# Kernel tuning notes

Measured on AMD Instinct MI355X. Metric: run time of the kernel, lower is better.

The kernel has to match this reference:

```python
import jax, jax.numpy as jnp
import numpy as np

N = 50000      # nodes
E = 800000     # edges (avg degree 16)
D = 128        # enc_input_dim
H = 4          # enc_num_heads
C = 32         # enc_hidden_dim (per head)
OUT = 64       # linear_output_dim
NEG_SLOPE = 0.2


def setup_inputs() -> dict:
    key = jax.random.key(0)
    ks = jax.random.split(key, 12)
    def glorot(k, shape, fan):
        return (jax.random.normal(k, shape, jnp.float32) / np.sqrt(fan)).astype(jnp.float32)
    x = jax.random.normal(ks[0], (N, D), jnp.float32)
    edge_index = jax.random.randint(ks[1], (2, E), 0, N, dtype=jnp.int64)
    # GAT layer 0: in=D, out=C per head, heads=H, concat -> H*C
    W0 = glorot(ks[2], (D, H * C), D)
    att_src0 = glorot(ks[3], (H, C), C)
    att_dst0 = glorot(ks[4], (H, C), C)
    b0 = jnp.zeros((H * C,), jnp.float32)
    # GAT layer 1: in=H*C, out=D, heads=1
    W1 = glorot(ks[5], (H * C, D), H * C)
    att_src1 = glorot(ks[6], (1, D), D)
    att_dst1 = glorot(ks[7], (1, D), D)
    b1 = jnp.zeros((D,), jnp.float32)
    # projection heads
    Wn = glorot(ks[8], (D, OUT), D)
    bn = jnp.zeros((OUT,), jnp.float32)
    We = glorot(ks[9], (D, OUT), D)
    be = jnp.zeros((OUT,), jnp.float32)
    return dict(x=x, edge_index=edge_index,
                W0=W0, att_src0=att_src0, att_dst0=att_dst0, b0=b0,
                W1=W1, att_src1=att_src1, att_dst1=att_dst1, b1=b1,
                Wn=Wn, bn=bn, We=We, be=be)


def gat_conv(x, src, dst, W, att_s, att_d, b):
    # PyG GATConv: project, per-head attention logits, LeakyReLU,
    # softmax over incoming edges per destination node, scatter-add aggregate.
    n = x.shape[0]
    heads, ch = att_s.shape
    xl = (x @ W).reshape(n, heads, ch)                       # [N,H,C]
    a_s = jnp.einsum('nhc,hc->nh', xl, att_s)                # [N,H]
    a_d = jnp.einsum('nhc,hc->nh', xl, att_d)                # [N,H]
    alpha = jax.nn.leaky_relu(a_s[src] + a_d[dst], NEG_SLOPE)  # [E',H]
    amax = jax.lax.stop_gradient(jax.ops.segment_max(alpha, dst, num_segments=n))
    ex = jnp.exp(alpha - amax[dst])
    denom = jax.ops.segment_sum(ex, dst, num_segments=n)
    w = ex / (denom[dst] + 1e-16)                            # [E',H]
    out = jax.ops.segment_sum(xl[src] * w[:, :, None], dst, num_segments=n)
    return out.reshape(n, heads * ch) + b


def reference(x, edge_index, W0, att_src0, att_dst0, b0,
              W1, att_src1, att_dst1, b1, Wn, bn, We, be):
    n = x.shape[0]
    loop = jnp.arange(n, dtype=edge_index.dtype)             # PyG add_self_loops
    src = jnp.concatenate([edge_index[0], loop])
    dst = jnp.concatenate([edge_index[1], loop])
    h = jax.nn.relu(gat_conv(x, src, dst, W0, att_src0, att_dst0, b0))
    h = jax.nn.relu(gat_conv(h, src, dst, W1, att_src1, att_dst1, b1))
    h_neighbor = h @ Wn + bn
    h_ego = x @ We + be
    return (h_ego, h_neighbor)
```

## Files before the change

kernel.cpp:

```cpp
#include <hip/hip_runtime.h>


#define LEAKY_SLOPE 0.2f
#define BUCKET_CAP 64

typedef __attribute__((ext_vector_type(8))) short s16x8;
typedef __attribute__((ext_vector_type(4))) float f32x4;
typedef __attribute__((ext_vector_type(2))) float f32x2;

static __device__ __forceinline__ unsigned short f2bf(float f)
{
    unsigned x = __float_as_uint(f);
    unsigned r = (x + 0x7fffu + ((x >> 16) & 1u)) >> 16;
    return (unsigned short)r;
}
static __device__ __forceinline__ float bfhi(unsigned u) { return __uint_as_float(u & 0xffff0000u); }
static __device__ __forceinline__ float bflo(unsigned u) { return __uint_as_float(u << 16); }
static __device__ __forceinline__ unsigned char f2fp8(float f)
{
    return (unsigned char)(__builtin_amdgcn_cvt_pk_fp8_f32(f, f, 0, false) & 0xff);
}

__global__ __launch_bounds__(256) void init_k(const float* __restrict__ W0,
                                              const float* __restrict__ W1,
                                              const float* __restrict__ Wn,
                                              const float* __restrict__ We,
                                              unsigned short* __restrict__ P0,
                                              unsigned short* __restrict__ P1,
                                              unsigned short* __restrict__ Pn,
                                              unsigned short* __restrict__ Pe)
{
    int idx = blockIdx.x * 256 + threadIdx.x;
    if (idx < 49152) {
        const float* S; unsigned short* D; int BN; int local;
        if (idx < 16384)      { S = W0; D = P0; BN = 128; local = idx; }
        else if (idx < 32768) { S = W1; D = P1; BN = 128; local = idx - 16384; }
        else if (idx < 40960) { S = Wn; D = Pn; BN = 64;  local = idx - 32768; }
        else                  { S = We; D = Pe; BN = 64;  local = idx - 40960; }
        int k = local / BN, nn = local % BN;
        D[(((k >> 3) * BN + nn) * 8) + (k & 7)] = f2bf(S[local]);
    }
}

static __device__ __forceinline__ void gemm128_body(int tile,
                                                    const float* __restrict__ Ab,
                                                    const unsigned short* __restrict__ Bp,
                                                    unsigned char* __restrict__ Cb,
                                                    const float* __restrict__ ats,
                                                    const float* __restrict__ atd,
                                                    float* __restrict__ a_s,
                                                    float* __restrict__ a_d, int n,
                                                    char* __restrict__ sm)
{
    constexpr int BN = 128;
    constexpr int APITCH = 144;
    constexpr int BPITCH = BN + 2;

    unsigned short* As = (unsigned short*)sm;
    unsigned short* Bs = (unsigned short*)(sm + 64 * APITCH * 2);

    const int t  = threadIdx.x;
    const int rb = tile * 64;

#pragma unroll
    for (int i = 0; i < 4; ++i) {
        int q = t + i * 256;
        int r = q >> 4;
        int c = (q & 15) * 8;
        int gr = rb + r;
        uint4 o = make_uint4(0u, 0u, 0u, 0u);
        if (gr < n) {
            const float* src = Ab + (size_t)gr * 128 + c;
            float4 v0 = *(const float4*)src;
            float4 v1 = *(const float4*)(src + 4);
            o.x = (unsigned)f2bf(v0.x) | ((unsigned)f2bf(v0.y) << 16);
            o.y = (unsigned)f2bf(v0.z) | ((unsigned)f2bf(v0.w) << 16);
            o.z = (unsigned)f2bf(v1.x) | ((unsigned)f2bf(v1.y) << 16);
            o.w = (unsigned)f2bf(v1.z) | ((unsigned)f2bf(v1.w) << 16);
        }
        *(uint4*)(As + r * APITCH + c) = o;
    }
#pragma unroll
    for (int i = 0; i < 8; ++i) {
        int ge = t + i * 256;
        int o = ge / BN, nn = ge % BN;
        *(float4*)(Bs + ((size_t)o * BPITCH + nn) * 8) = *(const float4*)(Bp + (size_t)ge * 8);
    }
    __syncthreads();

    const int w = t >> 6, lane = t & 63;
    const int m = lane & 15, quad = lane >> 4;
    const int wc = w & 1, wr = w >> 1;
    const int row0 = wr * 32;
    const int col0 = wc * 64;

    f32x4 acc[2][4];
#pragma unroll
    for (int rt = 0; rt < 2; ++rt)
#pragma unroll
        for (int c = 0; c < 4; ++c) acc[rt][c] = (f32x4){0.f, 0.f, 0.f, 0.f};

    s16x8 a[2][4];
#pragma unroll
    for (int rt = 0; rt < 2; ++rt)
#pragma unroll
        for (int kk = 0; kk < 4; ++kk)
            a[rt][kk] = *(const s16x8*)(As + (row0 + rt * 16 + m) * APITCH + kk * 32 + quad * 8);

#pragma unroll
    for (int kk = 0; kk < 4; ++kk)
#pragma unroll
        for (int c = 0; c < 4; ++c) {
            s16x8 b = *(const s16x8*)(Bs + ((size_t)(kk * 4 + quad) * BPITCH + col0 + c * 16 + m) * 8);
#pragma unroll
            for (int rt = 0; rt < 2; ++rt)
                acc[rt][c] = __builtin_amdgcn_mfma_f32_16x16x32_bf16(a[rt][kk], b, acc[rt][c], 0, 0, 0);
        }

#pragma unroll
    for (int rt = 0; rt < 2; ++rt)
#pragma unroll
        for (int c = 0; c < 4; ++c)
#pragma unroll
            for (int r = 0; r < 4; ++r) {
                int row = rb + row0 + rt * 16 + quad * 4 + r;
                int colg = col0 + c * 16 + m;
                if (row < n) Cb[(size_t)row * 128 + colg] = f2fp8(acc[rt][c][r]);
            }

    float atsv[4], atdv[4];
#pragma unroll
    for (int c = 0; c < 4; ++c) {
        atsv[c] = ats[col0 + c * 16 + m];
        atdv[c] = atd[col0 + c * 16 + m];
    }
#pragma unroll
    for (int rt = 0; rt < 2; ++rt)
#pragma unroll
        for (int r = 0; r < 4; ++r)
#pragma unroll
            for (int hb = 0; hb < 2; ++hb) {
                float ps = acc[rt][2*hb][r] * atsv[2*hb] + acc[rt][2*hb+1][r] * atsv[2*hb+1];
                float pd = acc[rt][2*hb][r] * atdv[2*hb] + acc[rt][2*hb+1][r] * atdv[2*hb+1];
#pragma unroll
                for (int off = 1; off < 16; off <<= 1) {
                    ps += __shfl_xor(ps, off);
                    pd += __shfl_xor(pd, off);
                }
                int row = rb + row0 + rt * 16 + quad * 4 + r;
                if (m == 0 && row < n) {
                    a_s[(size_t)row * 4 + 2*wc + hb] = ps;
                    a_d[(size_t)row * 4 + 2*wc + hb] = pd;
                }
            }
}

static __device__ __forceinline__ void proj64_body(int tile,
                                                   const float* __restrict__ Ab,
                                                   const unsigned short* __restrict__ Bp,
                                                   const float* __restrict__ bias,
                                                   float* __restrict__ Cf, int n,
                                                   char* __restrict__ sm)
{
    constexpr int BN = 64;
    constexpr int APITCH = 144;
    constexpr int BPITCH = BN + 2;

    unsigned short* As = (unsigned short*)sm;
    unsigned short* Bs = (unsigned short*)(sm + 64 * APITCH * 2);

    const int t  = threadIdx.x;
    const int rb = tile * 64;

#pragma unroll
    for (int i = 0; i < 4; ++i) {
        int q = t + i * 256;
        int r = q >> 4;
        int c = (q & 15) * 8;
        int gr = rb + r;
        uint4 o = make_uint4(0u, 0u, 0u, 0u);
        if (gr < n) {
            const float* src = Ab + (size_t)gr * 128 + c;
            float4 v0 = *(const float4*)src;
            float4 v1 = *(const float4*)(src + 4);
            o.x = (unsigned)f2bf(v0.x) | ((unsigned)f2bf(v0.y) << 16);
            o.y = (unsigned)f2bf(v0.z) | ((unsigned)f2bf(v0.w) << 16);
            o.z = (unsigned)f2bf(v1.x) | ((unsigned)f2bf(v1.y) << 16);
            o.w = (unsigned)f2bf(v1.z) | ((unsigned)f2bf(v1.w) << 16);
        }
        *(uint4*)(As + r * APITCH + c) = o;
    }
#pragma unroll
    for (int i = 0; i < 4; ++i) {
        int ge = t + i * 256;
        int o = ge / BN, nn = ge % BN;
        *(float4*)(Bs + ((size_t)o * BPITCH + nn) * 8) = *(const float4*)(Bp + (size_t)ge * 8);
    }
    __syncthreads();

    const int w = t >> 6, lane = t & 63;
    const int m = lane & 15, quad = lane >> 4;
    const int row0 = w * 16;

    f32x4 acc[4];
#pragma unroll
    for (int c = 0; c < 4; ++c) acc[c] = (f32x4){0.f, 0.f, 0.f, 0.f};

    s16x8 a[4];
#pragma unroll
    for (int kk = 0; kk < 4; ++kk)
        a[kk] = *(const s16x8*)(As + (row0 + m) * APITCH + kk * 32 + quad * 8);

#pragma unroll
    for (int kk = 0; kk < 4; ++kk)
#pragma unroll
        for (int c = 0; c < 4; ++c) {
            s16x8 b = *(const s16x8*)(Bs + ((size_t)(kk * 4 + quad) * BPITCH + c * 16 + m) * 8);
            acc[c] = __builtin_amdgcn_mfma_f32_16x16x32_bf16(a[kk], b, acc[c], 0, 0, 0);
        }

#pragma unroll
    for (int c = 0; c < 4; ++c)
#pragma unroll
        for (int r = 0; r < 4; ++r) {
            int row = rb + row0 + quad * 4 + r;
            int colg = c * 16 + m;
            if (row < n) Cf[(size_t)row * BN + colg] = acc[c][r] + bias[colg];
        }
}

__global__ __launch_bounds__(256) void build_k(const float* __restrict__ x,
                                               const unsigned short* __restrict__ P0,
                                               const unsigned short* __restrict__ Pe,
                                               unsigned char* __restrict__ xlb,
                                               const float* __restrict__ ats,
                                               const float* __restrict__ atd,
                                               float* __restrict__ a_s,
                                               float* __restrict__ a_d,
                                               const float* __restrict__ be,
                                               float* __restrict__ Ce,
                                               const int* __restrict__ ei,
                                               int* __restrict__ curs,
                                               unsigned short* __restrict__ col,
                                               int E, int n,
                                               int scatBlocks, int gemmBlocks)
{
    extern __shared__ char sm[];
    int b = blockIdx.x;
    if (b < scatBlocks) {
        int t8 = (b * 256 + threadIdx.x) * 8;
        if (t8 < E) {
            if ((E & 7) == 0) {
                int4 s0 = *(const int4*)(ei + t8);
                int4 s1 = *(const int4*)(ei + t8 + 4);
                int4 d0 = *(const int4*)(ei + E + t8);
                int4 d1 = *(const int4*)(ei + E + t8 + 4);
                int p0 = atomicAdd(&curs[d0.x << 4], 1);
                int p1 = atomicAdd(&curs[d0.y << 4], 1);
                int p2 = atomicAdd(&curs[d0.z << 4], 1);
                int p3 = atomicAdd(&curs[d0.w << 4], 1);
                int p4 = atomicAdd(&curs[d1.x << 4], 1);
                int p5 = atomicAdd(&curs[d1.y << 4], 1);
                int p6 = atomicAdd(&curs[d1.z << 4], 1);
                int p7 = atomicAdd(&curs[d1.w << 4], 1);
                if (p0 < BUCKET_CAP) col[(d0.x << 6) + p0] = (unsigned short)s0.x;
                if (p1 < BUCKET_CAP) col[(d0.y << 6) + p1] = (unsigned short)s0.y;
                if (p2 < BUCKET_CAP) col[(d0.z << 6) + p2] = (unsigned short)s0.z;
                if (p3 < BUCKET_CAP) col[(d0.w << 6) + p3] = (unsigned short)s0.w;
                if (p4 < BUCKET_CAP) col[(d1.x << 6) + p4] = (unsigned short)s1.x;
                if (p5 < BUCKET_CAP) col[(d1.y << 6) + p5] = (unsigned short)s1.y;
                if (p6 < BUCKET_CAP) col[(d1.z << 6) + p6] = (unsigned short)s1.z;
                if (p7 < BUCKET_CAP) col[(d1.w << 6) + p7] = (unsigned short)s1.w;
            } else {
                int lim = (t8 + 8 < E) ? t8 + 8 : E;
                for (int e = t8; e < lim; ++e) {
                    int s = ei[e], d = ei[E + e];
                    int p = atomicAdd(&curs[d << 4], 1);
                    if (p < BUCKET_CAP) col[(d << 6) + p] = (unsigned short)s;
                }
            }
        }
    } else if (b < scatBlocks + gemmBlocks) {
        gemm128_body(b - scatBlocks, x, P0, xlb, ats, atd, a_s, a_d, n, sm);
    } else {
        proj64_body(b - scatBlocks - gemmBlocks, x, Pe, be, Ce, n, sm);
    }
}

template<int LAYER>
__global__ __launch_bounds__(256) void agg_mv_k(const unsigned char* __restrict__ xin,
                                                const float* __restrict__ asi,
                                                const float* __restrict__ adi,
                                                const int* __restrict__ curs,
                                                const unsigned short* __restrict__ col,
                                                const float* __restrict__ bpre,
                                                const unsigned short* __restrict__ Wp,
                                                const float* __restrict__ ats,
                                                const float* __restrict__ atd,
                                                unsigned char* __restrict__ xlo,
                                                float* __restrict__ aso,
                                                float* __restrict__ ado,
                                                const float* __restrict__ bpost,
                                                float* __restrict__ outf,
                                                int n)
{
    constexpr int H  = (LAYER == 0) ? 4 : 1;
    constexpr int BN = (LAYER == 0) ? 128 : 64;

    __shared__ unsigned short hrow[16 * 128];
    __shared__ float smS[64], smD[64];

    const int t = threadIdx.x;

    const int nd   = t >> 4;
    const int L16  = t & 15;
    const int lane = t & 63;
    const int gb   = lane & 48;
    const int node = blockIdx.x * 16 + nd;
    const int h    = (LAYER == 0) ? (L16 >> 2) : 0;

    if (node < n) {
        float c0=0.f,c1=0.f,c2=0.f,c3=0.f,c4=0.f,c5=0.f,c6=0.f,c7=0.f,den=0.f;
        float ad = adi[(size_t)node * H + h];
        int m = curs[node << 4];
        if (m > BUCKET_CAP) m = BUCKET_CAP;
        const unsigned char* xbase = xin + L16 * 8;
        const int p0 = node << 6;

        int cvu = 0;
        for (int j = 0; j < m; j += 8) {
            if ((j & 15) == 0) cvu = col[p0 + j + L16];
            int cnt = m - j; if (cnt > 8) cnt = 8;
            int sq[8]; float as8[8]; uint2 uv[8];
#pragma unroll
            for (int q = 0; q < 8; ++q) {
                int idx = (q < cnt) ? (j + q) : j;
                sq[q] = __shfl(cvu, gb + (idx & 15));
            }
#pragma unroll
            for (int q = 0; q < 8; ++q) as8[q] = asi[(size_t)sq[q] * H + h];
#pragma unroll
            for (int q = 0; q < 8; ++q) uv[q] = *(const uint2*)(xbase + (size_t)sq[q] * 128);
#pragma unroll
            for (int q = 0; q < 8; ++q) {
                float al = as8[q] + ad;
                al = (al >= 0.f) ? al : LEAKY_SLOPE * al;
                float wq = (q < cnt) ? __expf(al) : 0.f;
                f32x2 pa = __builtin_amdgcn_cvt_pk_f32_fp8((int)uv[q].x, false);
                f32x2 pb = __builtin_amdgcn_cvt_pk_f32_fp8((int)uv[q].x, true);
                f32x2 pc = __builtin_amdgcn_cvt_pk_f32_fp8((int)uv[q].y, false);
                f32x2 pd2 = __builtin_amdgcn_cvt_pk_f32_fp8((int)uv[q].y, true);
                c0 = fmaf(wq, pa[0], c0); c1 = fmaf(wq, pa[1], c1);
                c2 = fmaf(wq, pb[0], c2); c3 = fmaf(wq, pb[1], c3);
                c4 = fmaf(wq, pc[0], c4); c5 = fmaf(wq, pc[1], c5);
                c6 = fmaf(wq, pd2[0], c6); c7 = fmaf(wq, pd2[1], c7);
                den += wq;
            }
        }
        {
            float sv = asi[(size_t)node * H + h];
            float al = sv + ad;
            al = (al >= 0.f) ? al : LEAKY_SLOPE * al;
            float ws = __expf(al);
            uint2 uvs = *(const uint2*)(xbase + (size_t)node * 128);
            f32x2 pa = __builtin_amdgcn_cvt_pk_f32_fp8((int)uvs.x, false);
            f32x2 pb = __builtin_amdgcn_cvt_pk_f32_fp8((int)uvs.x, true);
            f32x2 pc = __builtin_amdgcn_cvt_pk_f32_fp8((int)uvs.y, false);
            f32x2 pd2 = __builtin_amdgcn_cvt_pk_f32_fp8((int)uvs.y, true);
            c0 = fmaf(ws, pa[0], c0); c1 = fmaf(ws, pa[1], c1);
            c2 = fmaf(ws, pb[0], c2); c3 = fmaf(ws, pb[1], c3);
            c4 = fmaf(ws, pc[0], c4); c5 = fmaf(ws, pc[1], c5);
            c6 = fmaf(ws, pd2[0], c6); c7 = fmaf(ws, pd2[1], c7);
            den += ws;
        }
        float inv = 1.0f / (den + 1e-16f);
        const float* bp = bpre + L16 * 8;
        float h0v = fmaxf(fmaf(c0, inv, bp[0]), 0.f);
        float h1v = fmaxf(fmaf(c1, inv, bp[1]), 0.f);
        float h2v = fmaxf(fmaf(c2, inv, bp[2]), 0.f);
        float h3v = fmaxf(fmaf(c3, inv, bp[3]), 0.f);
        float h4v = fmaxf(fmaf(c4, inv, bp[4]), 0.f);
        float h5v = fmaxf(fmaf(c5, inv, bp[5]), 0.f);
        float h6v = fmaxf(fmaf(c6, inv, bp[6]), 0.f);
        float h7v = fmaxf(fmaf(c7, inv, bp[7]), 0.f);
        uint4 hv;
        hv.x = (unsigned)f2bf(h0v) | ((unsigned)f2bf(h1v) << 16);
        hv.y = (unsigned)f2bf(h2v) | ((unsigned)f2bf(h3v) << 16);
        hv.z = (unsigned)f2bf(h4v) | ((unsigned)f2bf(h5v) << 16);
        hv.w = (unsigned)f2bf(h6v) | ((unsigned)f2bf(h7v) << 16);
        *(uint4*)(hrow + nd * 128 + L16 * 8) = hv;
    } else {
        *(uint4*)(hrow + nd * 128 + L16 * 8) = make_uint4(0u, 0u, 0u, 0u);
    }

    __syncthreads();

    const int w    = t >> 6;
    const int m16  = lane & 15;
    const int quad = lane >> 4;

    s16x8 afr[4];
#pragma unroll
    for (int kk = 0; kk < 4; ++kk)
        afr[kk] = *(const s16x8*)(hrow + m16 * 128 + kk * 32 + quad * 8);

    if (LAYER == 0) {
        f32x4 acc[2];
        acc[0] = (f32x4){0.f, 0.f, 0.f, 0.f};
        acc[1] = (f32x4){0.f, 0.f, 0.f, 0.f};
#pragma unroll
        for (int kk = 0; kk < 4; ++kk)
#pragma unroll
            for (int ct = 0; ct < 2; ++ct) {
                int colg = (w * 2 + ct) * 16 + m16;
                s16x8 b = *(const s16x8*)(Wp + ((size_t)(kk * 4 + quad) * BN + colg) * 8);
                acc[ct] = __builtin_amdgcn_mfma_f32_16x16x32_bf16(afr[kk], b, acc[ct], 0, 0, 0);
            }
#pragma unroll
        for (int r = 0; r < 4; ++r) {
            int gnode = blockIdx.x * 16 + quad * 4 + r;
            float ps = 0.f, pd = 0.f;
#pragma unroll
            for (int ct = 0; ct < 2; ++ct) {
                int colg = (w * 2 + ct) * 16 + m16;
                float v = acc[ct][r];
                if (gnode < n) xlo[(size_t)gnode * 128 + colg] = f2fp8(v);
                ps = fmaf(v, ats[colg], ps);
                pd = fmaf(v, atd[colg], pd);
            }
#pragma unroll
            for (int off = 1; off < 16; off <<= 1) {
                ps += __shfl_xor(ps, off);
                pd += __shfl_xor(pd, off);
            }
            if (m16 == 0) {
                smS[(quad * 4 + r) * 4 + w] = ps;
                smD[(quad * 4 + r) * 4 + w] = pd;
            }
        }
        __syncthreads();
        if (t < 16) {
            int gnode = blockIdx.x * 16 + t;
            if (gnode < n) {
                aso[gnode] = smS[t * 4] + smS[t * 4 + 1] + smS[t * 4 + 2] + smS[t * 4 + 3];
                ado[gnode] = smD[t * 4] + smD[t * 4 + 1] + smD[t * 4 + 2] + smD[t * 4 + 3];
            }
        }
    } else {
        f32x4 acc = (f32x4){0.f, 0.f, 0.f, 0.f};
        int colg = w * 16 + m16;
#pragma unroll
        for (int kk = 0; kk < 4; ++kk) {
            s16x8 b = *(const s16x8*)(Wp + ((size_t)(kk * 4 + quad) * BN + colg) * 8);
            acc = __builtin_amdgcn_mfma_f32_16x16x32_bf16(afr[kk], b, acc, 0, 0, 0);
        }
        float bv = bpost[colg];
#pragma unroll
        for (int r = 0; r < 4; ++r) {
            int gnode = blockIdx.x * 16 + quad * 4 + r;
            if (gnode < n) outf[(size_t)gnode * 64 + colg] = acc[r] + bv;
        }
    }
}

extern "C" void kernel_launch(void* const* d_in, const int* in_sizes, int n_in,
                              void* d_out, int out_size, void* d_ws, size_t ws_size,
                              hipStream_t stream)
{
    const float* x   = (const float*)d_in[0];
    const int*   ei  = (const int*)d_in[1];
    const float* W0  = (const float*)d_in[2];
    const float* as0 = (const float*)d_in[3];
    const float* ad0 = (const float*)d_in[4];
    const float* b0  = (const float*)d_in[5];
    const float* W1  = (const float*)d_in[6];
    const float* as1 = (const float*)d_in[7];
    const float* ad1 = (const float*)d_in[8];
    const float* b1  = (const float*)d_in[9];
    const float* Wn  = (const float*)d_in[10];
    const float* bn  = (const float*)d_in[11];
    const float* We  = (const float*)d_in[12];
    const float* be  = (const float*)d_in[13];

    const int n  = in_sizes[0] / 128;
    const int E  = in_sizes[1] / 2;
    float* out = (float*)d_out;

    char* w = (char*)d_ws;
    auto carve = [&](size_t bytes) -> void* {
        void* p = (void*)w;
        w += (bytes + 255) & ~(size_t)255;
        return p;
    };
    unsigned char* xlb = (unsigned char*)carve((size_t)n * 128);
    unsigned char* hb  = (unsigned char*)carve((size_t)n * 128);
    float* a_s0 = (float*)carve((size_t)n * 4 * 4);
    float* a_d0 = (float*)carve((size_t)n * 4 * 4);
    float* a_s1 = (float*)carve((size_t)n * 4);
    float* a_d1 = (float*)carve((size_t)n * 4);
    int*   curs = (int*)carve((size_t)n * 16 * 4);
    unsigned short* colv = (unsigned short*)carve((size_t)n * BUCKET_CAP * 2);
    unsigned short* P0 = (unsigned short*)carve(16384 * 2);
    unsigned short* P1 = (unsigned short*)carve(16384 * 2);
    unsigned short* Pn = (unsigned short*)carve(8192 * 2);
    unsigned short* Pe = (unsigned short*)carve(8192 * 2);

    const int gN64  = (n + 63) / 64;
    const int gB16  = (n + 15) / 16;
    const int gScat = ((E + 7) / 8 + 255) / 256;

    constexpr int GEMM_SM = 64 * 144 * 2 + 16 * 130 * 8 * 2;

    hipMemsetAsync(curs, 0, (size_t)n * 16 * 4, stream);
    init_k<<<192, 256, 0, stream>>>(W0, W1, Wn, We, P0, P1, Pn, Pe);

    build_k<<<gScat + 2 * gN64, 256, GEMM_SM, stream>>>(x, P0, Pe, xlb, as0, ad0,
                                                        a_s0, a_d0, be, out,
                                                        ei, curs, colv, E, n,
                                                        gScat, gN64);

    agg_mv_k<0><<<gB16, 256, 0, stream>>>(xlb, a_s0, a_d0, curs, colv, b0,
                                          P1, as1, ad1,
                                          hb, a_s1, a_d1,
                                          nullptr, nullptr, n);

    agg_mv_k<1><<<gB16, 256, 0, stream>>>(hb, a_s1, a_d1, curs, colv, b1,
                                          Pn, nullptr, nullptr,
                                          nullptr, nullptr, nullptr,
                                          bn, out + (size_t)n * 64, n);
}
```

Baseline: 201.9 us.

## Recompute attention logits from fp8 features in aggregation and drop init kernel

Removes the separate weight-packing kernel. W0/We are now converted to bf16 directly inside the GEMM tile loads, and W1/Wn packing moves into extra blocks of build_k. The per-node a_s/a_d attention arrays are dropped: the aggregation kernel recomputes both logits from the gathered fp8 feature rows with per-lane dot products and shuffle reductions. This saves a launch and the a_s/a_d stores and gathers, but adds ALU and shuffle work per edge and computes logits from fp8-quantized features, which changes precision.

```diff
diff --git a/kernel.cpp b/kernel.cpp
--- a/kernel.cpp
+++ b/kernel.cpp
@@ -14,43 +14,25 @@
     unsigned r = (x + 0x7fffu + ((x >> 16) & 1u)) >> 16;
     return (unsigned short)r;
 }
-static __device__ __forceinline__ float bfhi(unsigned u) { return __uint_as_float(u & 0xffff0000u); }
-static __device__ __forceinline__ float bflo(unsigned u) { return __uint_as_float(u << 16); }
 static __device__ __forceinline__ unsigned char f2fp8(float f)
 {
     return (unsigned char)(__builtin_amdgcn_cvt_pk_fp8_f32(f, f, 0, false) & 0xff);
 }
-
-__global__ __launch_bounds__(256) void init_k(const float* __restrict__ W0,
-                                              const float* __restrict__ W1,
-                                              const float* __restrict__ Wn,
-                                              const float* __restrict__ We,
-                                              unsigned short* __restrict__ P0,
-                                              unsigned short* __restrict__ P1,
-                                              unsigned short* __restrict__ Pn,
-                                              unsigned short* __restrict__ Pe)
-{
-    int idx = blockIdx.x * 256 + threadIdx.x;
-    if (idx < 49152) {
-        const float* S; unsigned short* D; int BN; int local;
-        if (idx < 16384)      { S = W0; D = P0; BN = 128; local = idx; }
-        else if (idx < 32768) { S = W1; D = P1; BN = 128; local = idx - 16384; }
-        else if (idx < 40960) { S = Wn; D = Pn; BN = 64;  local = idx - 32768; }
-        else                  { S = We; D = Pe; BN = 64;  local = idx - 40960; }
-        int k = local / BN, nn = local % BN;
-        D[(((k >> 3) * BN + nn) * 8) + (k & 7)] = f2bf(S[local]);
-    }
+static __device__ __forceinline__ void dq8(uint2 u, float* v)
+{
+    f32x2 a = __builtin_amdgcn_cvt_pk_f32_fp8((int)u.x, false);
+    f32x2 b = __builtin_amdgcn_cvt_pk_f32_fp8((int)u.x, true);
+    f32x2 c = __builtin_amdgcn_cvt_pk_f32_fp8((int)u.y, false);
+    f32x2 d = __builtin_amdgcn_cvt_pk_f32_fp8((int)u.y, true);
+    v[0] = a[0]; v[1] = a[1]; v[2] = b[0]; v[3] = b[1];
+    v[4] = c[0]; v[5] = c[1]; v[6] = d[0]; v[7] = d[1];
 }
 
 static __device__ __forceinline__ void gemm128_body(int tile,
                                                     const float* __restrict__ Ab,
-                                                    const unsigned short* __restrict__ Bp,
+                                                    const float* __restrict__ W,
                                                     unsigned char* __restrict__ Cb,
-                                                    const float* __restrict__ ats,
-                                                    const float* __restrict__ atd,
-                                                    float* __restrict__ a_s,
-                                                    float* __restrict__ a_d, int n,
-                                                    char* __restrict__ sm)
+                                                    int n, char* __restrict__ sm)
 {
     constexpr int BN = 128;
     constexpr int APITCH = 144;
@@ -83,8 +65,12 @@
 #pragma unroll
     for (int i = 0; i < 8; ++i) {
         int ge = t + i * 256;
-        int o = ge / BN, nn = ge % BN;
-        *(float4*)(Bs + ((size_t)o * BPITCH + nn) * 8) = *(const float4*)(Bp + (size_t)ge * 8);
+        int o = ge >> 7, nn = ge & 127;
+        const float* src = W + (size_t)(o * 8) * 128 + nn;
+        unsigned short pk[8];
+#pragma unroll
+        for (int j = 0; j < 8; ++j) pk[j] = f2bf(src[(size_t)j * 128]);
+        *(uint4*)(Bs + ((size_t)o * BPITCH + nn) * 8) = *(const uint4*)pk;
     }
     __syncthreads();
 
@@ -127,37 +113,11 @@
                 int colg = col0 + c * 16 + m;
                 if (row < n) Cb[(size_t)row * 128 + colg] = f2fp8(acc[rt][c][r]);
             }
-
-    float atsv[4], atdv[4];
-#pragma unroll
-    for (int c = 0; c < 4; ++c) {
-        atsv[c] = ats[col0 + c * 16 + m];
-        atdv[c] = atd[col0 + c * 16 + m];
-    }
-#pragma unroll
-    for (int rt = 0; rt < 2; ++rt)
-#pragma unroll
-        for (int r = 0; r < 4; ++r)
-#pragma unroll
-            for (int hb = 0; hb < 2; ++hb) {
-                float ps = acc[rt][2*hb][r] * atsv[2*hb] + acc[rt][2*hb+1][r] * atsv[2*hb+1];
-                float pd = acc[rt][2*hb][r] * atdv[2*hb] + acc[rt][2*hb+1][r] * atdv[2*hb+1];
-#pragma unroll
-                for (int off = 1; off < 16; off <<= 1) {
-                    ps += __shfl_xor(ps, off);
-                    pd += __shfl_xor(pd, off);
-                }
-                int row = rb + row0 + rt * 16 + quad * 4 + r;
-                if (m == 0 && row < n) {
-                    a_s[(size_t)row * 4 + 2*wc + hb] = ps;
-                    a_d[(size_t)row * 4 + 2*wc + hb] = pd;
-                }
-            }
 }
 
 static __device__ __forceinline__ void proj64_body(int tile,
                                                    const float* __restrict__ Ab,
-                                                   const unsigned short* __restrict__ Bp,
+                                                   const float* __restrict__ W,
                                                    const float* __restrict__ bias,
                                                    float* __restrict__ Cf, int n,
                                                    char* __restrict__ sm)
@@ -193,8 +153,12 @@
 #pragma unroll
     for (int i = 0; i < 4; ++i) {
         int ge = t + i * 256;
-        int o = ge / BN, nn = ge % BN;
-        *(float4*)(Bs + ((size_t)o * BPITCH + nn) * 8) = *(const float4*)(Bp + (size_t)ge * 8);
+        int o = ge >> 6, nn = ge & 63;
+        const float* src = W + (size_t)(o * 8) * 64 + nn;
+        unsigned short pk[8];
+#pragma unroll
+        for (int j = 0; j < 8; ++j) pk[j] = f2bf(src[(size_t)j * 64]);
+        *(uint4*)(Bs + ((size_t)o * BPITCH + nn) * 8) = *(const uint4*)pk;
     }
     __syncthreads();
 
@@ -230,18 +194,18 @@
 }
 
 __global__ __launch_bounds__(256) void build_k(const float* __restrict__ x,
-                                               const unsigned short* __restrict__ P0,
-                                               const unsigned short* __restrict__ Pe,
+                                               const float* __restrict__ W0,
+                                               const float* __restrict__ We,
+                                               const float* __restrict__ W1,
+                                               const float* __restrict__ Wn,
                                                unsigned char* __restrict__ xlb,
-                                               const float* __restrict__ ats,
-                                               const float* __restrict__ atd,
-                                               float* __restrict__ a_s,
-                                               float* __restrict__ a_d,
                                                const float* __restrict__ be,
                                                float* __restrict__ Ce,
                                                const int* __restrict__ ei,
                                                int* __restrict__ curs,
                                                unsigned short* __restrict__ col,
+                                               unsigned short* __restrict__ P1,
+                                               unsigned short* __restrict__ Pn,
                                                int E, int n,
                                                int scatBlocks, int gemmBlocks)
 {
@@ -281,97 +245,107 @@
             }
         }
     } else if (b < scatBlocks + gemmBlocks) {
-        gemm128_body(b - scatBlocks, x, P0, xlb, ats, atd, a_s, a_d, n, sm);
+        gemm128_body(b - scatBlocks, x, W0, xlb, n, sm);
+    } else if (b < scatBlocks + 2 * gemmBlocks) {
+        proj64_body(b - scatBlocks - gemmBlocks, x, We, be, Ce, n, sm);
     } else {
-        proj64_body(b - scatBlocks - gemmBlocks, x, Pe, be, Ce, n, sm);
+        int idx = (b - scatBlocks - 2 * gemmBlocks) * 256 + threadIdx.x;
+        if (idx < 24576) {
+            const float* S; unsigned short* D; int BN2; int local;
+            if (idx < 16384) { S = W1; D = P1; BN2 = 128; local = idx; }
+            else             { S = Wn; D = Pn; BN2 = 64;  local = idx - 16384; }
+            int k = local / BN2, nn = local % BN2;
+            D[(((k >> 3) * BN2 + nn) * 8) + (k & 7)] = f2bf(S[local]);
+        }
     }
 }
 
 template<int LAYER>
 __global__ __launch_bounds__(256) void agg_mv_k(const unsigned char* __restrict__ xin,
-                                                const float* __restrict__ asi,
-                                                const float* __restrict__ adi,
                                                 const int* __restrict__ curs,
                                                 const unsigned short* __restrict__ col,
+                                                const float* __restrict__ att_s,
+                                                const float* __restrict__ att_d,
                                                 const float* __restrict__ bpre,
                                                 const unsigned short* __restrict__ Wp,
-                                                const float* __restrict__ ats,
-                                                const float* __restrict__ atd,
                                                 unsigned char* __restrict__ xlo,
-                                                float* __restrict__ aso,
-                                                float* __restrict__ ado,
                                                 const float* __restrict__ bpost,
                                                 float* __restrict__ outf,
                                                 int n)
 {
-    constexpr int H  = (LAYER == 0) ? 4 : 1;
     constexpr int BN = (LAYER == 0) ? 128 : 64;
+    constexpr int RW = (LAYER == 0) ? 4 : 16;
 
     __shared__ unsigned short hrow[16 * 128];
-    __shared__ float smS[64], smD[64];
 
     const int t = threadIdx.x;
-
     const int nd   = t >> 4;
     const int L16  = t & 15;
     const int lane = t & 63;
     const int gb   = lane & 48;
     const int node = blockIdx.x * 16 + nd;
-    const int h    = (LAYER == 0) ? (L16 >> 2) : 0;
+
+    const float4 sa = *(const float4*)(att_s + L16 * 8);
+    const float4 sb = *(const float4*)(att_s + L16 * 8 + 4);
+    const float4 da = *(const float4*)(att_d + L16 * 8);
+    const float4 db = *(const float4*)(att_d + L16 * 8 + 4);
 
     if (node < n) {
-        float c0=0.f,c1=0.f,c2=0.f,c3=0.f,c4=0.f,c5=0.f,c6=0.f,c7=0.f,den=0.f;
-        float ad = adi[(size_t)node * H + h];
+        const unsigned char* xbase = xin + L16 * 8;
+
+        uint2 us = *(const uint2*)(xbase + (size_t)node * 128);
+        float vs[8]; dq8(us, vs);
+        float pss = vs[0]*sa.x + vs[1]*sa.y + vs[2]*sa.z + vs[3]*sa.w
+                  + vs[4]*sb.x + vs[5]*sb.y + vs[6]*sb.z + vs[7]*sb.w;
+        float pdd = vs[0]*da.x + vs[1]*da.y + vs[2]*da.z + vs[3]*da.w
+                  + vs[4]*db.x + vs[5]*db.y + vs[6]*db.z + vs[7]*db.w;
+        pss += __shfl_xor(pss, 1); pss += __shfl_xor(pss, 2);
+        pdd += __shfl_xor(pdd, 1); pdd += __shfl_xor(pdd, 2);
+        if (RW == 16) {
+            pss += __shfl_xor(pss, 4); pss += __shfl_xor(pss, 8);
+            pdd += __shfl_xor(pdd, 4); pdd += __shfl_xor(pdd, 8);
+        }
+        const float adv = pdd;
+
+        float als = pss + adv;
+        als = (als >= 0.f) ? als : LEAKY_SLOPE * als;
+        float ws = __expf(als);
+        float c0 = ws*vs[0], c1 = ws*vs[1], c2 = ws*vs[2], c3 = ws*vs[3];
+        float c4 = ws*vs[4], c5 = ws*vs[5], c6 = ws*vs[6], c7 = ws*vs[7];
+        float den = ws;
+
         int m = curs[node << 4];
         if (m > BUCKET_CAP) m = BUCKET_CAP;
-        const unsigned char* xbase = xin + L16 * 8;
         const int p0 = node << 6;
 
         int cvu = 0;
         for (int j = 0; j < m; j += 8) {
             if ((j & 15) == 0) cvu = col[p0 + j + L16];
             int cnt = m - j; if (cnt > 8) cnt = 8;
-            int sq[8]; float as8[8]; uint2 uv[8];
+            int sq[8]; uint2 uv[8];
 #pragma unroll
             for (int q = 0; q < 8; ++q) {
                 int idx = (q < cnt) ? (j + q) : j;
                 sq[q] = __shfl(cvu, gb + (idx & 15));
             }
 #pragma unroll
-            for (int q = 0; q < 8; ++q) as8[q] = asi[(size_t)sq[q] * H + h];
-#pragma unroll
             for (int q = 0; q < 8; ++q) uv[q] = *(const uint2*)(xbase + (size_t)sq[q] * 128);
 #pragma unroll
             for (int q = 0; q < 8; ++q) {
-                float al = as8[q] + ad;
+                float v[8]; dq8(uv[q], v);
+                float ps = v[0]*sa.x + v[1]*sa.y + v[2]*sa.z + v[3]*sa.w
+                         + v[4]*sb.x + v[5]*sb.y + v[6]*sb.z + v[7]*sb.w;
+                ps += __shfl_xor(ps, 1); ps += __shfl_xor(ps, 2);
+                if (RW == 16) { ps += __shfl_xor(ps, 4); ps += __shfl_xor(ps, 8); }
+                float al = ps + adv;
                 al = (al >= 0.f) ? al : LEAKY_SLOPE * al;
                 float wq = (q < cnt) ? __expf(al) : 0.f;
-                f32x2 pa = __builtin_amdgcn_cvt_pk_f32_fp8((int)uv[q].x, false);
-                f32x2 pb = __builtin_amdgcn_cvt_pk_f32_fp8((int)uv[q].x, true);
-                f32x2 pc = __builtin_amdgcn_cvt_pk_f32_fp8((int)uv[q].y, false);
-                f32x2 pd2 = __builtin_amdgcn_cvt_pk_f32_fp8((int)uv[q].y, true);
-                c0 = fmaf(wq, pa[0], c0); c1 = fmaf(wq, pa[1], c1);
-                c2 = fmaf(wq, pb[0], c2); c3 = fmaf(wq, pb[1], c3);
-                c4 = fmaf(wq, pc[0], c4); c5 = fmaf(wq, pc[1], c5);
-                c6 = fmaf(wq, pd2[0], c6); c7 = fmaf(wq, pd2[1], c7);
+                c0 = fmaf(wq, v[0], c0); c1 = fmaf(wq, v[1], c1);
+                c2 = fmaf(wq, v[2], c2); c3 = fmaf(wq, v[3], c3);
+                c4 = fmaf(wq, v[4], c4); c5 = fmaf(wq, v[5], c5);
+                c6 = fmaf(wq, v[6], c6); c7 = fmaf(wq, v[7], c7);
                 den += wq;
             }
-        }
-        {
-            float sv = asi[(size_t)node * H + h];
-            float al = sv + ad;
-            al = (al >= 0.f) ? al : LEAKY_SLOPE * al;
-            float ws = __expf(al);
-            uint2 uvs = *(const uint2*)(xbase + (size_t)node * 128);
-            f32x2 pa = __builtin_amdgcn_cvt_pk_f32_fp8((int)uvs.x, false);
-            f32x2 pb = __builtin_amdgcn_cvt_pk_f32_fp8((int)uvs.x, true);
-            f32x2 pc = __builtin_amdgcn_cvt_pk_f32_fp8((int)uvs.y, false);
-            f32x2 pd2 = __builtin_amdgcn_cvt_pk_f32_fp8((int)uvs.y, true);
-            c0 = fmaf(ws, pa[0], c0); c1 = fmaf(ws, pa[1], c1);
-            c2 = fmaf(ws, pb[0], c2); c3 = fmaf(ws, pb[1], c3);
-            c4 = fmaf(ws, pc[0], c4); c5 = fmaf(ws, pc[1], c5);
-            c6 = fmaf(ws, pd2[0], c6); c7 = fmaf(ws, pd2[1], c7);
-            den += ws;
         }
         float inv = 1.0f / (den + 1e-16f);
         const float* bp = bpre + L16 * 8;
@@ -419,31 +393,12 @@
 #pragma unroll
         for (int r = 0; r < 4; ++r) {
             int gnode = blockIdx.x * 16 + quad * 4 + r;
-            float ps = 0.f, pd = 0.f;
-#pragma unroll
-            for (int ct = 0; ct < 2; ++ct) {
-                int colg = (w * 2 + ct) * 16 + m16;
-                float v = acc[ct][r];
-                if (gnode < n) xlo[(size_t)gnode * 128 + colg] = f2fp8(v);
-                ps = fmaf(v, ats[colg], ps);
-                pd = fmaf(v, atd[colg], pd);
-            }
-#pragma unroll
-            for (int off = 1; off < 16; off <<= 1) {
-                ps += __shfl_xor(ps, off);
-                pd += __shfl_xor(pd, off);
-            }
-            if (m16 == 0) {
-                smS[(quad * 4 + r) * 4 + w] = ps;
-                smD[(quad * 4 + r) * 4 + w] = pd;
-            }
-        }
-        __syncthreads();
-        if (t < 16) {
-            int gnode = blockIdx.x * 16 + t;
             if (gnode < n) {
-                aso[gnode] = smS[t * 4] + smS[t * 4 + 1] + smS[t * 4 + 2] + smS[t * 4 + 3];
-                ado[gnode] = smD[t * 4] + smD[t * 4 + 1] + smD[t * 4 + 2] + smD[t * 4 + 3];
+#pragma unroll
+                for (int ct = 0; ct < 2; ++ct) {
+                    int colg = (w * 2 + ct) * 16 + m16;
+                    xlo[(size_t)gnode * 128 + colg] = f2fp8(acc[ct][r]);
+                }
             }
         }
     } else {
@@ -494,16 +449,10 @@
     };
     unsigned char* xlb = (unsigned char*)carve((size_t)n * 128);
     unsigned char* hb  = (unsigned char*)carve((size_t)n * 128);
-    float* a_s0 = (float*)carve((size_t)n * 4 * 4);
-    float* a_d0 = (float*)carve((size_t)n * 4 * 4);
-    float* a_s1 = (float*)carve((size_t)n * 4);
-    float* a_d1 = (float*)carve((size_t)n * 4);
     int*   curs = (int*)carve((size_t)n * 16 * 4);
     unsigned short* colv = (unsigned short*)carve((size_t)n * BUCKET_CAP * 2);
-    unsigned short* P0 = (unsigned short*)carve(16384 * 2);
     unsigned short* P1 = (unsigned short*)carve(16384 * 2);
     unsigned short* Pn = (unsigned short*)carve(8192 * 2);
-    unsigned short* Pe = (unsigned short*)carve(8192 * 2);
 
     const int gN64  = (n + 63) / 64;
     const int gB16  = (n + 15) / 16;
@@ -512,20 +461,16 @@
     constexpr int GEMM_SM = 64 * 144 * 2 + 16 * 130 * 8 * 2;
 
     hipMemsetAsync(curs, 0, (size_t)n * 16 * 4, stream);
-    init_k<<<192, 256, 0, stream>>>(W0, W1, Wn, We, P0, P1, Pn, Pe);
-
-    build_k<<<gScat + 2 * gN64, 256, GEMM_SM, stream>>>(x, P0, Pe, xlb, as0, ad0,
-                                                        a_s0, a_d0, be, out,
-                                                        ei, curs, colv, E, n,
-                                                        gScat, gN64);
-
-    agg_mv_k<0><<<gB16, 256, 0, stream>>>(xlb, a_s0, a_d0, curs, colv, b0,
-                                          P1, as1, ad1,
-                                          hb, a_s1, a_d1,
-                                          nullptr, nullptr, n);
-
-    agg_mv_k<1><<<gB16, 256, 0, stream>>>(hb, a_s1, a_d1, curs, colv, b1,
-                                          Pn, nullptr, nullptr,
-                                          nullptr, nullptr, nullptr,
-                                          bn, out + (size_t)n * 64, n);
-}
+
+    build_k<<<gScat + 2 * gN64 + 96, 256, GEMM_SM, stream>>>(x, W0, We, W1, Wn,
+                                                             xlb, be, out,
+                                                             ei, curs, colv,
+                                                             P1, Pn, E, n,
+                                                             gScat, gN64);
+
+    agg_mv_k<0><<<gB16, 256, 0, stream>>>(xlb, curs, colv, as0, ad0, b0,
+                                          P1, hb, nullptr, nullptr, n);
+
+    agg_mv_k<1><<<gB16, 256, 0, stream>>>(hb, curs, colv, as1, ad1, b1,
+                                          Pn, nullptr, bn, out + (size_t)n * 64, n);
+}
```

New measurement: 221.8 us. 9.8% more time.
